# Kernel optimization log

Measured on AMD Instinct MI355X. Metric: run time of the kernel, lower is better.

The kernel has to match this reference:

```python
import jax, jax.numpy as jnp
import numpy as np

B = 4096          # graphs
NPG = 50          # nodes per graph
N = B * NPG       # total nodes
E = 819200        # edges
C = 128           # hidden_channels
T = 2048          # num_tools


def setup_inputs() -> dict:
    key = jax.random.key(0)
    ks = jax.random.split(key, 12)
    s = 0.1
    return {
        "x": jax.random.randint(ks[0], (N, 1), 0, T, dtype=jnp.int32),
        "edge_index": jax.random.randint(ks[1], (2, E), 0, N, dtype=jnp.int32),
        "batch": (jnp.arange(N, dtype=jnp.int32) // NPG).astype(jnp.int32),
        "num_graphs": B,
        "embedding": jax.random.normal(ks[2], (T, C), jnp.float32) * s,
        "w_ih": jax.random.normal(ks[3], (3 * C, C), jnp.float32) * s,
        "w_hh": jax.random.normal(ks[4], (3 * C, C), jnp.float32) * s,
        "w1": jax.random.normal(ks[5], (C, C), jnp.float32) * s,
        "w2": jax.random.normal(ks[6], (C, C), jnp.float32) * s,
        "b2": jax.random.normal(ks[7], (C,), jnp.float32) * s,
        "wq": jax.random.normal(ks[8], (C, C), jnp.float32) * s,
        "bq": jax.random.normal(ks[9], (C,), jnp.float32) * s,
        "wt": jax.random.normal(ks[10], (C, 2 * C), jnp.float32) * s,
    }


def reference(x, edge_index, batch, num_graphs, embedding, w_ih, w_hh,
              w1, w2, b2, wq, bq, wt):
    n = x.shape[0]
    # embedding lookup (dropout2d is identity at eval)
    emb = embedding[x[:, 0]]                                   # [N, C]

    # --- GatedGraphConv: scatter-add of source features to targets ---
    src, dst = edge_index[0], edge_index[1]
    m = jax.ops.segment_sum(emb[src], dst, num_segments=n)     # [N, C]

    # --- GRUCell(m, emb), no bias ---
    gi = m @ w_ih.T                                            # [N, 3C]
    gh = emb @ w_hh.T                                          # [N, 3C]
    i_r, i_z, i_n = jnp.split(gi, 3, axis=1)
    h_r, h_z, h_n = jnp.split(gh, 3, axis=1)
    r = jax.nn.sigmoid(i_r + h_r)
    z = jax.nn.sigmoid(i_z + h_z)
    ncand = jnp.tanh(i_n + r * h_n)
    h = (1.0 - z) * ncand + z * emb                            # [N, C]

    # --- ragged segment attention readout ---
    counts = jax.ops.segment_sum(jnp.ones_like(batch), batch,
                                 num_segments=num_graphs)      # [B]
    last_idx = jnp.cumsum(counts) - 1                          # [B]
    w_l = h[last_idx]                                          # [B, C] last node per graph
    w_g_r = w_l[batch]                                         # [N, C] broadcast to nodes
    q1 = w_g_r @ w1.T
    q2 = h @ w2.T + b2
    alpha = jax.nn.sigmoid(q1 + q2) @ wq.T + bq                # [N, C]
    w_g = jax.ops.segment_sum(alpha * h, batch,
                              num_segments=num_graphs)         # [B, C]

    w = jnp.concatenate([w_l, w_g], axis=1) @ wt.T             # [B, C]
    logits = w @ embedding.T                                   # [B, T]
    return logits
```

## Files before the change

kernel.cpp:

```cpp
#include <hip/hip_runtime.h>
#include <hip/hip_bf16.h>

#define NN 204800
#define EE 819200
#define BB 4096
#define NPG 50
#define CC 128
#define TT 2048
#define BINCAP 32

typedef __attribute__((ext_vector_type(8))) short short8;
typedef __attribute__((ext_vector_type(4))) float f32x4;

__device__ __forceinline__ short f2bf(float f) {
    union { float f; unsigned u; } v; v.f = f;
    unsigned r = (v.u + 0x7FFFu + ((v.u >> 16) & 1u)) >> 16;
    return (short)r;
}
__device__ __forceinline__ float bf2f(short s) {
    union { float f; unsigned u; } v;
    v.u = ((unsigned)(unsigned short)s) << 16;
    return v.f;
}
__device__ __forceinline__ float sigf(float x) { return 1.0f / (1.0f + __expf(-x)); }
__device__ __forceinline__ float tanh_fast(float x) {
    x = fminf(fmaxf(x, -15.0f), 15.0f);
    float e = __expf(2.0f * x);
    return 1.0f - 2.0f / (e + 1.0f);
}

__global__ void prep_small(const float* __restrict__ emb, const float* __restrict__ w1,
                           const float* __restrict__ w2, const float* __restrict__ wq,
                           const float* __restrict__ wt,
                           __hip_bfloat16* __restrict__ embbf, __hip_bfloat16* __restrict__ w1bf,
                           __hip_bfloat16* __restrict__ w2bf, __hip_bfloat16* __restrict__ wqbf,
                           __hip_bfloat16* __restrict__ wtbf) {
    int i = blockIdx.x * 256 + threadIdx.x;
    if (i < TT * CC) embbf[i] = __float2bfloat16(emb[i]);
    if (i < CC * CC) {
        w1bf[i] = __float2bfloat16(w1[i]);
        w2bf[i] = __float2bfloat16(w2[i]);
        wqbf[i] = __float2bfloat16(wq[i]);
    }
    if (i < CC * 2 * CC) wtbf[i] = __float2bfloat16(wt[i]);
}

__global__ __launch_bounds__(256) void build_tables(const float* __restrict__ emb,
                                                    const float* __restrict__ w_ih,
                                                    const float* __restrict__ w_hh,
                                                    __hip_bfloat16* __restrict__ G_ih,
                                                    __hip_bfloat16* __restrict__ G_hh) {
    __shared__ float wch[CC][CC + 1];
    __shared__ float et[16][CC];
    int t = threadIdx.x;
    int tokbase = blockIdx.x * 16;
    int chunk = blockIdx.y;
    const float* w = (chunk < 3) ? w_ih : w_hh;
    __hip_bfloat16* G = (chunk < 3) ? G_ih : G_hh;
    int jbase = (chunk % 3) * CC;
    for (int idx = t; idx < CC * CC; idx += 256) {
        int j = idx >> 7, k = idx & 127;
        wch[j][k] = w[(jbase + j) * CC + k];
    }
    for (int idx = t; idx < 16 * CC; idx += 256) {
        int tok = idx >> 7, k = idx & 127;
        et[tok][k] = emb[(tokbase + tok) * CC + k];
    }
    __syncthreads();
    int j = t & 127, grp = t >> 7;
    float acc[8];
#pragma unroll
    for (int u = 0; u < 8; u++) acc[u] = 0.f;
    for (int k = 0; k < CC; k++) {
        float wv = wch[j][k];
#pragma unroll
        for (int u = 0; u < 8; u++) acc[u] += et[grp * 8 + u][k] * wv;
    }
#pragma unroll
    for (int u = 0; u < 8; u++)
        G[(tokbase + grp * 8 + u) * 384 + jbase + j] = __float2bfloat16(acc[u]);
}

__global__ void fill_bins(const int* __restrict__ ei, const int* __restrict__ x,
                          int* __restrict__ deg, int* __restrict__ bins) {
    int e = blockIdx.x * 256 + threadIdx.x;
    int d = ei[EE + e], s = ei[e];
    int pos = atomicAdd(&deg[d], 1);
    bins[(size_t)d * BINCAP + pos] = x[s];
}

__global__ __launch_bounds__(256) void gru_kernel(
    const int* __restrict__ x, const int* __restrict__ deg,
    const int* __restrict__ bins,
    const __hip_bfloat16* __restrict__ G_ih, const __hip_bfloat16* __restrict__ G_hh,
    const float* __restrict__ emb,
    __hip_bfloat16* __restrict__ hbf) {
    int nid = blockIdx.x * 16 + (threadIdx.x >> 4);
    int j = threadIdx.x & 15;
    int tok = x[nid];
    int dg = deg[nid];
    const int* bin = bins + (size_t)nid * BINCAP;
    float ir[8], iz[8], inn[8];
#pragma unroll
    for (int p = 0; p < 8; p++) { ir[p] = 0.f; iz[p] = 0.f; inn[p] = 0.f; }
    for (int c = 0; c < dg; c += 4) {
        int4 tq = *(const int4*)&bin[c];
        int tks[4] = {tq.x, tq.y, tq.z, tq.w};
#pragma unroll
        for (int u = 0; u < 4; u++) {
            if (c + u < dg) {
                int st = tks[u];
                const short8* gp = (const short8*)(G_ih + (size_t)st * 384);
                short8 a = gp[j];
                short8 b = gp[16 + j];
                short8 c2 = gp[32 + j];
#pragma unroll
                for (int p = 0; p < 8; p++) {
                    ir[p]  += bf2f(a[p]);
                    iz[p]  += bf2f(b[p]);
                    inn[p] += bf2f(c2[p]);
                }
            }
        }
    }
    const short8* hp = (const short8*)(G_hh + (size_t)tok * 384);
    short8 hr = hp[j], hz = hp[16 + j], hn = hp[32 + j];
    const float4* ep = (const float4*)(emb + (size_t)tok * CC + j * 8);
    float4 ev0 = ep[0], ev1 = ep[1];
    float evs[8] = {ev0.x, ev0.y, ev0.z, ev0.w, ev1.x, ev1.y, ev1.z, ev1.w};
    short8 hv;
#pragma unroll
    for (int p = 0; p < 8; p++) {
        float r  = sigf(ir[p] + bf2f(hr[p]));
        float z  = sigf(iz[p] + bf2f(hz[p]));
        float nc = tanh_fast(inn[p] + r * bf2f(hn[p]));
        float h  = (1.f - z) * nc + z * evs[p];
        hv[p] = f2bf(h);
    }
    ((short8*)hbf)[nid * 16 + j] = hv;
}

__global__ __launch_bounds__(256) void q1_kernel(
    const __hip_bfloat16* __restrict__ hbf, const __hip_bfloat16* __restrict__ w1bf,
    const float* __restrict__ b2,
    float* __restrict__ q1_all, __hip_bfloat16* __restrict__ w_lbf) {
    int t = threadIdx.x;
    int gbase = blockIdx.x * 64;
    int wave = t >> 6, lane = t & 63;
    int mrow = lane & 15, quad = lane >> 4;
    int g = gbase + wave * 16 + mrow;

    short8 afr[4];
#pragma unroll
    for (int kt = 0; kt < 4; kt++) {
        afr[kt] = *(const short8*)(hbf + ((size_t)g * NPG + NPG - 1) * CC + kt * 32 + quad * 8);
        *(short8*)(w_lbf + (size_t)g * CC + kt * 32 + quad * 8) = afr[kt];
    }
    f32x4 acc[8];
#pragma unroll
    for (int nt = 0; nt < 8; nt++) {
        float bv = b2[nt * 16 + mrow];
        acc[nt] = (f32x4){bv, bv, bv, bv};
    }
#pragma unroll
    for (int kt = 0; kt < 4; kt++) {
#pragma unroll
        for (int nt = 0; nt < 8; nt++) {
            const short8* bp = (const short8*)(w1bf + (nt * 16 + mrow) * CC + kt * 32 + quad * 8);
            acc[nt] = __builtin_amdgcn_mfma_f32_16x16x32_bf16(afr[kt], *bp, acc[nt], 0, 0, 0);
        }
    }
#pragma unroll
    for (int nt = 0; nt < 8; nt++)
#pragma unroll
        for (int r = 0; r < 4; r++)
            q1_all[(size_t)(gbase + wave * 16 + quad * 4 + r) * CC + nt * 16 + mrow] = acc[nt][r];
}

__global__ __launch_bounds__(256, 4) void node_attn(
    const __hip_bfloat16* __restrict__ hbf, const float* __restrict__ q1_all,
    const __hip_bfloat16* __restrict__ w2bf, const __hip_bfloat16* __restrict__ wqbf,
    const float* __restrict__ bq,
    float* __restrict__ w_gf) {
    __shared__ short hsb[64][CC + 8];
    __shared__ short ssb[64][CC + 8];
    int rb = blockIdx.x * 64;
    int t = threadIdx.x;

    const short8* hsrc = (const short8*)(hbf + (size_t)rb * CC);
#pragma unroll
    for (int it = 0; it < 4; it++) {
        int idx = it * 256 + t;
        *(short8*)&hsb[idx >> 4][(idx & 15) * 8] = hsrc[idx];
    }
    __syncthreads();

    int wave = t >> 6, lane = t & 63;
    int mrow = lane & 15, quad = lane >> 4;
    int colb = wave * 32;

    f32x4 acc[4][2];
#pragma unroll
    for (int rt = 0; rt < 4; rt++)
#pragma unroll
        for (int n = 0; n < 2; n++) acc[rt][n] = (f32x4){0.f, 0.f, 0.f, 0.f};
    {
        short8 bw2[2][4];
#pragma unroll
        for (int n = 0; n < 2; n++)
#pragma unroll
            for (int kt = 0; kt < 4; kt++)
                bw2[n][kt] = *(const short8*)(w2bf + (size_t)(colb + n * 16 + mrow) * CC + kt * 32 + quad * 8);
#pragma unroll
        for (int kt = 0; kt < 4; kt++)
#pragma unroll
            for (int rt = 0; rt < 4; rt++) {
                short8 af = *(const short8*)&hsb[rt * 16 + mrow][kt * 32 + quad * 8];
#pragma unroll
                for (int n = 0; n < 2; n++)
                    acc[rt][n] = __builtin_amdgcn_mfma_f32_16x16x32_bf16(af, bw2[n][kt], acc[rt][n], 0, 0, 0);
            }
    }
#pragma unroll
    for (int rt = 0; rt < 4; rt++)
#pragma unroll
        for (int n = 0; n < 2; n++)
#pragma unroll
            for (int r = 0; r < 4; r++) {
                int rowl = rt * 16 + quad * 4 + r;
                int col = colb + n * 16 + mrow;
                int g = (rb + rowl) / 50;
                ssb[rowl][col] = f2bf(sigf(acc[rt][n][r] + q1_all[(size_t)g * CC + col]));
            }
    __syncthreads();

    f32x4 acd[4][2];
    short8 bwq[2][4];
#pragma unroll
    for (int n = 0; n < 2; n++) {
        float bv = bq[colb + n * 16 + mrow];
#pragma unroll
        for (int rt = 0; rt < 4; rt++) acd[rt][n] = (f32x4){bv, bv, bv, bv};
#pragma unroll
        for (int kt = 0; kt < 4; kt++)
            bwq[n][kt] = *(const short8*)(wqbf + (size_t)(colb + n * 16 + mrow) * CC + kt * 32 + quad * 8);
    }
#pragma unroll
    for (int kt = 0; kt < 4; kt++)
#pragma unroll
        for (int rt = 0; rt < 4; rt++) {
            short8 af = *(const short8*)&ssb[rt * 16 + mrow][kt * 32 + quad * 8];
#pragma unroll
            for (int n = 0; n < 2; n++)
                acd[rt][n] = __builtin_amdgcn_mfma_f32_16x16x32_bf16(af, bwq[n][kt], acd[rt][n], 0, 0, 0);
        }
    int g0 = rb / 50;
    int gmax = (rb + 63) / 50;
#pragma unroll
    for (int n = 0; n < 2; n++) {
        int col = colb + n * 16 + mrow;
        float ps0 = 0.f, ps1 = 0.f, ps2 = 0.f;
#pragma unroll
        for (int rt = 0; rt < 4; rt++)
#pragma unroll
            for (int r = 0; r < 4; r++) {
                int rowl = rt * 16 + quad * 4 + r;
                int gg = (rb + rowl) / 50;
                float v = acd[rt][n][r] * bf2f(hsb[rowl][col]);
                ps0 += (gg == g0)     ? v : 0.f;
                ps1 += (gg == g0 + 1) ? v : 0.f;
                ps2 += (gg == g0 + 2) ? v : 0.f;
            }
        ps0 += __shfl_xor(ps0, 16, 64); ps0 += __shfl_xor(ps0, 32, 64);
        ps1 += __shfl_xor(ps1, 16, 64); ps1 += __shfl_xor(ps1, 32, 64);
        ps2 += __shfl_xor(ps2, 16, 64); ps2 += __shfl_xor(ps2, 32, 64);
        if (quad == 0) {
            atomicAdd(&w_gf[(size_t)g0 * CC + col], ps0);
            if (g0 + 1 <= gmax) atomicAdd(&w_gf[(size_t)(g0 + 1) * CC + col], ps1);
            if (g0 + 2 <= gmax) atomicAdd(&w_gf[(size_t)(g0 + 2) * CC + col], ps2);
        }
    }
}

__global__ __launch_bounds__(256) void wvec_kernel(
    const __hip_bfloat16* __restrict__ w_lbf, const float* __restrict__ w_gf,
    const __hip_bfloat16* __restrict__ wtbf,
    __hip_bfloat16* __restrict__ wvecbf) {
    int t = threadIdx.x;
    int gbase = blockIdx.x * 64;
    int wave = t >> 6, lane = t & 63;
    int mrow = lane & 15, quad = lane >> 4;
    int grow = gbase + wave * 16 + mrow;

    f32x4 acc[8];
#pragma unroll
    for (int nt = 0; nt < 8; nt++) acc[nt] = (f32x4){0.f, 0.f, 0.f, 0.f};
#pragma unroll
    for (int kt = 0; kt < 8; kt++) {
        short8 af;
        if (kt < 4) {
            af = *(const short8*)(w_lbf + (size_t)grow * CC + kt * 32 + quad * 8);
        } else {
            const float* ws = w_gf + (size_t)grow * CC + (kt - 4) * 32 + quad * 8;
            float4 v0 = *(const float4*)ws, v1 = *(const float4*)(ws + 4);
            af[0] = f2bf(v0.x); af[1] = f2bf(v0.y); af[2] = f2bf(v0.z); af[3] = f2bf(v0.w);
            af[4] = f2bf(v1.x); af[5] = f2bf(v1.y); af[6] = f2bf(v1.z); af[7] = f2bf(v1.w);
        }
#pragma unroll
        for (int nt = 0; nt < 8; nt++) {
            const short8* bp = (const short8*)(wtbf + (nt * 16 + mrow) * 256 + kt * 32 + quad * 8);
            acc[nt] = __builtin_amdgcn_mfma_f32_16x16x32_bf16(af, *bp, acc[nt], 0, 0, 0);
        }
    }
#pragma unroll
    for (int nt = 0; nt < 8; nt++)
#pragma unroll
        for (int r = 0; r < 4; r++)
            wvecbf[(size_t)(gbase + wave * 16 + quad * 4 + r) * CC + nt * 16 + mrow] =
                __float2bfloat16(acc[nt][r]);
}

__global__ __launch_bounds__(256) void logits_kernel(
    const __hip_bfloat16* __restrict__ wvecbf, const __hip_bfloat16* __restrict__ embbf,
    float* __restrict__ out) {
    __shared__ short avs[64][CC + 8];
    int t = threadIdx.x;
    int gbase = blockIdx.x * 64;
    int tbase = blockIdx.y * 128;

    const short8* asrc = (const short8*)(wvecbf + (size_t)gbase * CC);
#pragma unroll
    for (int it = 0; it < 4; it++) {
        int idx = it * 256 + t;
        *(short8*)&avs[idx >> 4][(idx & 15) * 8] = asrc[idx];
    }
    __syncthreads();

    int wave = t >> 6, lane = t & 63;
    int mrow = lane & 15, quad = lane >> 4;

    f32x4 acc3[8];
#pragma unroll
    for (int nt = 0; nt < 8; nt++) acc3[nt] = (f32x4){0.f, 0.f, 0.f, 0.f};
#pragma unroll
    for (int kt = 0; kt < 4; kt++) {
        short8 af = *(const short8*)&avs[wave * 16 + mrow][kt * 32 + quad * 8];
#pragma unroll
        for (int nt = 0; nt < 8; nt++) {
            const short8* bp = (const short8*)(embbf + (size_t)(tbase + nt * 16 + mrow) * CC + kt * 32 + quad * 8);
            acc3[nt] = __builtin_amdgcn_mfma_f32_16x16x32_bf16(af, *bp, acc3[nt], 0, 0, 0);
        }
    }
#pragma unroll
    for (int nt = 0; nt < 8; nt++)
#pragma unroll
        for (int r = 0; r < 4; r++) {
            int grow2 = gbase + wave * 16 + quad * 4 + r;
            int tok = tbase + nt * 16 + mrow;
            out[(size_t)grow2 * TT + tok] = acc3[nt][r];
        }
}

extern "C" void kernel_launch(void* const* d_in, const int* in_sizes, int n_in,
                              void* d_out, int out_size, void* d_ws, size_t ws_size,
                              hipStream_t stream) {
    const int* x     = (const int*)d_in[0];
    const int* ei    = (const int*)d_in[1];
    const float* emb = (const float*)d_in[4];
    const float* w_ih = (const float*)d_in[5];
    const float* w_hh = (const float*)d_in[6];
    const float* w1  = (const float*)d_in[7];
    const float* w2  = (const float*)d_in[8];
    const float* b2  = (const float*)d_in[9];
    const float* wq  = (const float*)d_in[10];
    const float* bq  = (const float*)d_in[11];
    const float* wt  = (const float*)d_in[12];
    float* out = (float*)d_out;

    char* ws = (char*)d_ws;
    size_t off = 0;
    auto alloc = [&](size_t b) { void* p = ws + off; off += (b + 255) & ~(size_t)255; return p; };
    __hip_bfloat16* G_ih  = (__hip_bfloat16*)alloc((size_t)TT * 384 * 2);
    __hip_bfloat16* G_hh  = (__hip_bfloat16*)alloc((size_t)TT * 384 * 2);
    __hip_bfloat16* embbf = (__hip_bfloat16*)alloc((size_t)TT * CC * 2);
    __hip_bfloat16* w1bf  = (__hip_bfloat16*)alloc((size_t)CC * CC * 2);
    __hip_bfloat16* w2bf  = (__hip_bfloat16*)alloc((size_t)CC * CC * 2);
    __hip_bfloat16* wqbf  = (__hip_bfloat16*)alloc((size_t)CC * CC * 2);
    __hip_bfloat16* wtbf  = (__hip_bfloat16*)alloc((size_t)CC * 256 * 2);
    int* deg              = (int*)alloc((size_t)NN * 4);
    int* bins             = (int*)alloc((size_t)NN * BINCAP * 4);
    __hip_bfloat16* w_lbf = (__hip_bfloat16*)alloc((size_t)BB * CC * 2);
    float* w_gf           = (float*)alloc((size_t)BB * CC * 4);
    float* q1_all         = (float*)alloc((size_t)BB * CC * 4);
    __hip_bfloat16* wvecbf= (__hip_bfloat16*)alloc((size_t)BB * CC * 2);
    __hip_bfloat16* hbf   = (__hip_bfloat16*)alloc((size_t)NN * CC * 2);

    hipMemsetAsync(deg, 0, (size_t)NN * 4, stream);
    hipMemsetAsync(w_gf, 0, (size_t)BB * CC * 4, stream);
    prep_small<<<1024, 256, 0, stream>>>(emb, w1, w2, wq, wt, embbf, w1bf, w2bf, wqbf, wtbf);
    build_tables<<<dim3(TT / 16, 6), 256, 0, stream>>>(emb, w_ih, w_hh, G_ih, G_hh);
    fill_bins<<<EE / 256, 256, 0, stream>>>(ei, x, deg, bins);
    gru_kernel<<<NN / 16, 256, 0, stream>>>(x, deg, bins, G_ih, G_hh, emb, hbf);
    q1_kernel<<<BB / 64, 256, 0, stream>>>(hbf, w1bf, b2, q1_all, w_lbf);
    node_attn<<<NN / 64, 256, 0, stream>>>(hbf, q1_all, w2bf, wqbf, bq, w_gf);
    wvec_kernel<<<BB / 64, 256, 0, stream>>>(w_lbf, w_gf, wtbf, wvecbf);
    logits_kernel<<<dim3(BB / 64, TT / 128), 256, 0, stream>>>(wvecbf, embbf, out);
}
```

Before: 308.8 us.

## Build GRU tables with MFMA, branchless gather, and cache q1 in LDS

Replaces the scalar fp32 FMA kernel that builds the per-token GRU gate tables with a bf16 MFMA kernel. The weights and embeddings are converted to bf16 in prep_small first. The GRU gather loop becomes branchless by pointing out-of-range slots at an extra zeroed table row. node_attn stages the three relevant q1 rows and each node's graph index in shared memory instead of doing per-element global loads and divisions. Table precision drops from an fp32 dot product to bf16 inputs, and the launch order changes.

Result: no change. 304.3 us (-1.5%).

```diff
diff --git a/kernel.cpp b/kernel.cpp
--- a/kernel.cpp
+++ b/kernel.cpp
@@ -31,10 +31,12 @@
 
 __global__ void prep_small(const float* __restrict__ emb, const float* __restrict__ w1,
                            const float* __restrict__ w2, const float* __restrict__ wq,
-                           const float* __restrict__ wt,
+                           const float* __restrict__ wt, const float* __restrict__ w_ih,
+                           const float* __restrict__ w_hh,
                            __hip_bfloat16* __restrict__ embbf, __hip_bfloat16* __restrict__ w1bf,
                            __hip_bfloat16* __restrict__ w2bf, __hip_bfloat16* __restrict__ wqbf,
-                           __hip_bfloat16* __restrict__ wtbf) {
+                           __hip_bfloat16* __restrict__ wtbf, __hip_bfloat16* __restrict__ w_ihbf,
+                           __hip_bfloat16* __restrict__ w_hhbf) {
     int i = blockIdx.x * 256 + threadIdx.x;
     if (i < TT * CC) embbf[i] = __float2bfloat16(emb[i]);
     if (i < CC * CC) {
@@ -43,42 +45,65 @@
         wqbf[i] = __float2bfloat16(wq[i]);
     }
     if (i < CC * 2 * CC) wtbf[i] = __float2bfloat16(wt[i]);
-}
-
-__global__ __launch_bounds__(256) void build_tables(const float* __restrict__ emb,
-                                                    const float* __restrict__ w_ih,
-                                                    const float* __restrict__ w_hh,
-                                                    __hip_bfloat16* __restrict__ G_ih,
-                                                    __hip_bfloat16* __restrict__ G_hh) {
-    __shared__ float wch[CC][CC + 1];
-    __shared__ float et[16][CC];
+    if (i < 3 * CC * CC) {
+        w_ihbf[i] = __float2bfloat16(w_ih[i]);
+        w_hhbf[i] = __float2bfloat16(w_hh[i]);
+    }
+}
+
+__global__ __launch_bounds__(256) void build_tables_mfma(
+    const __hip_bfloat16* __restrict__ embbf,
+    const __hip_bfloat16* __restrict__ w_ihbf, const __hip_bfloat16* __restrict__ w_hhbf,
+    __hip_bfloat16* __restrict__ G_ih, __hip_bfloat16* __restrict__ G_hh) {
+    __shared__ short at[64][CC + 8];
     int t = threadIdx.x;
-    int tokbase = blockIdx.x * 16;
+    int tokbase = blockIdx.x * 64;
     int chunk = blockIdx.y;
-    const float* w = (chunk < 3) ? w_ih : w_hh;
+    const __hip_bfloat16* wsel = (chunk < 3) ? w_ihbf : w_hhbf;
     __hip_bfloat16* G = (chunk < 3) ? G_ih : G_hh;
     int jbase = (chunk % 3) * CC;
-    for (int idx = t; idx < CC * CC; idx += 256) {
-        int j = idx >> 7, k = idx & 127;
-        wch[j][k] = w[(jbase + j) * CC + k];
-    }
-    for (int idx = t; idx < 16 * CC; idx += 256) {
-        int tok = idx >> 7, k = idx & 127;
-        et[tok][k] = emb[(tokbase + tok) * CC + k];
+
+    const short8* asrc = (const short8*)(embbf + (size_t)tokbase * CC);
+#pragma unroll
+    for (int it = 0; it < 4; it++) {
+        int idx = it * 256 + t;
+        *(short8*)&at[idx >> 4][(idx & 15) * 8] = asrc[idx];
     }
     __syncthreads();
-    int j = t & 127, grp = t >> 7;
-    float acc[8];
-#pragma unroll
-    for (int u = 0; u < 8; u++) acc[u] = 0.f;
-    for (int k = 0; k < CC; k++) {
-        float wv = wch[j][k];
-#pragma unroll
-        for (int u = 0; u < 8; u++) acc[u] += et[grp * 8 + u][k] * wv;
-    }
-#pragma unroll
-    for (int u = 0; u < 8; u++)
-        G[(tokbase + grp * 8 + u) * 384 + jbase + j] = __float2bfloat16(acc[u]);
+
+    int wave = t >> 6, lane = t & 63;
+    int mrow = lane & 15, quad = lane >> 4;
+    int colb = wave * 32;
+
+    f32x4 acc[4][2];
+#pragma unroll
+    for (int rt = 0; rt < 4; rt++)
+#pragma unroll
+        for (int n = 0; n < 2; n++) acc[rt][n] = (f32x4){0.f, 0.f, 0.f, 0.f};
+    short8 bw[2][4];
+#pragma unroll
+    for (int n = 0; n < 2; n++)
+#pragma unroll
+        for (int kt = 0; kt < 4; kt++)
+            bw[n][kt] = *(const short8*)(wsel + (size_t)(jbase + colb + n * 16 + mrow) * CC + kt * 32 + quad * 8);
+#pragma unroll
+    for (int kt = 0; kt < 4; kt++)
+#pragma unroll
+        for (int rt = 0; rt < 4; rt++) {
+            short8 af = *(const short8*)&at[rt * 16 + mrow][kt * 32 + quad * 8];
+#pragma unroll
+            for (int n = 0; n < 2; n++)
+                acc[rt][n] = __builtin_amdgcn_mfma_f32_16x16x32_bf16(af, bw[n][kt], acc[rt][n], 0, 0, 0);
+        }
+#pragma unroll
+    for (int rt = 0; rt < 4; rt++)
+#pragma unroll
+        for (int n = 0; n < 2; n++)
+#pragma unroll
+            for (int r = 0; r < 4; r++) {
+                int tok = tokbase + rt * 16 + quad * 4 + r;
+                G[(size_t)tok * 384 + jbase + colb + n * 16 + mrow] = __float2bfloat16(acc[rt][n][r]);
+            }
 }
 
 __global__ void fill_bins(const int* __restrict__ ei, const int* __restrict__ x,
@@ -108,18 +133,16 @@
         int tks[4] = {tq.x, tq.y, tq.z, tq.w};
 #pragma unroll
         for (int u = 0; u < 4; u++) {
-            if (c + u < dg) {
-                int st = tks[u];
-                const short8* gp = (const short8*)(G_ih + (size_t)st * 384);
-                short8 a = gp[j];
-                short8 b = gp[16 + j];
-                short8 c2 = gp[32 + j];
-#pragma unroll
-                for (int p = 0; p < 8; p++) {
-                    ir[p]  += bf2f(a[p]);
-                    iz[p]  += bf2f(b[p]);
-                    inn[p] += bf2f(c2[p]);
-                }
+            int st = (c + u < dg) ? tks[u] : TT;
+            const short8* gp = (const short8*)(G_ih + (size_t)st * 384);
+            short8 a = gp[j];
+            short8 b = gp[16 + j];
+            short8 c2 = gp[32 + j];
+#pragma unroll
+            for (int p = 0; p < 8; p++) {
+                ir[p]  += bf2f(a[p]);
+                iz[p]  += bf2f(b[p]);
+                inn[p] += bf2f(c2[p]);
             }
         }
     }
@@ -184,7 +207,10 @@
     float* __restrict__ w_gf) {
     __shared__ short hsb[64][CC + 8];
     __shared__ short ssb[64][CC + 8];
+    __shared__ float q1s[3][CC];
+    __shared__ int gidx[64];
     int rb = blockIdx.x * 64;
+    int g0 = rb / 50;
     int t = threadIdx.x;
 
     const short8* hsrc = (const short8*)(hbf + (size_t)rb * CC);
@@ -193,6 +219,11 @@
         int idx = it * 256 + t;
         *(short8*)&hsb[idx >> 4][(idx & 15) * 8] = hsrc[idx];
     }
+    if (t < 64) gidx[t] = (rb + t) / 50 - g0;
+    for (int idx = t; idx < 3 * CC; idx += 256) {
+        int gg = g0 + (idx >> 7);
+        q1s[idx >> 7][idx & 127] = (gg < BB) ? q1_all[(size_t)gg * CC + (idx & 127)] : 0.f;
+    }
     __syncthreads();
 
     int wave = t >> 6, lane = t & 63;
@@ -224,14 +255,15 @@
 #pragma unroll
     for (int rt = 0; rt < 4; rt++)
 #pragma unroll
-        for (int n = 0; n < 2; n++)
-#pragma unroll
-            for (int r = 0; r < 4; r++) {
-                int rowl = rt * 16 + quad * 4 + r;
+        for (int r = 0; r < 4; r++) {
+            int rowl = rt * 16 + quad * 4 + r;
+            int gi_ = gidx[rowl];
+#pragma unroll
+            for (int n = 0; n < 2; n++) {
                 int col = colb + n * 16 + mrow;
-                int g = (rb + rowl) / 50;
-                ssb[rowl][col] = f2bf(sigf(acc[rt][n][r] + q1_all[(size_t)g * CC + col]));
+                ssb[rowl][col] = f2bf(sigf(acc[rt][n][r] + q1s[gi_][col]));
             }
+        }
     __syncthreads();
 
     f32x4 acd[4][2];
@@ -254,8 +286,6 @@
             for (int n = 0; n < 2; n++)
                 acd[rt][n] = __builtin_amdgcn_mfma_f32_16x16x32_bf16(af, bwq[n][kt], acd[rt][n], 0, 0, 0);
         }
-    int g0 = rb / 50;
-    int gmax = (rb + 63) / 50;
 #pragma unroll
     for (int n = 0; n < 2; n++) {
         int col = colb + n * 16 + mrow;
@@ -265,19 +295,19 @@
 #pragma unroll
             for (int r = 0; r < 4; r++) {
                 int rowl = rt * 16 + quad * 4 + r;
-                int gg = (rb + rowl) / 50;
+                int gi_ = gidx[rowl];
                 float v = acd[rt][n][r] * bf2f(hsb[rowl][col]);
-                ps0 += (gg == g0)     ? v : 0.f;
-                ps1 += (gg == g0 + 1) ? v : 0.f;
-                ps2 += (gg == g0 + 2) ? v : 0.f;
+                ps0 += (gi_ == 0) ? v : 0.f;
+                ps1 += (gi_ == 1) ? v : 0.f;
+                ps2 += (gi_ == 2) ? v : 0.f;
             }
         ps0 += __shfl_xor(ps0, 16, 64); ps0 += __shfl_xor(ps0, 32, 64);
         ps1 += __shfl_xor(ps1, 16, 64); ps1 += __shfl_xor(ps1, 32, 64);
         ps2 += __shfl_xor(ps2, 16, 64); ps2 += __shfl_xor(ps2, 32, 64);
         if (quad == 0) {
             atomicAdd(&w_gf[(size_t)g0 * CC + col], ps0);
-            if (g0 + 1 <= gmax) atomicAdd(&w_gf[(size_t)(g0 + 1) * CC + col], ps1);
-            if (g0 + 2 <= gmax) atomicAdd(&w_gf[(size_t)(g0 + 2) * CC + col], ps2);
+            atomicAdd(&w_gf[(size_t)(g0 + 1) * CC + col], ps1);
+            if (g0 + 2 < BB) atomicAdd(&w_gf[(size_t)(g0 + 2) * CC + col], ps2);
         }
     }
 }
@@ -380,13 +410,15 @@
     char* ws = (char*)d_ws;
     size_t off = 0;
     auto alloc = [&](size_t b) { void* p = ws + off; off += (b + 255) & ~(size_t)255; return p; };
-    __hip_bfloat16* G_ih  = (__hip_bfloat16*)alloc((size_t)TT * 384 * 2);
+    __hip_bfloat16* G_ih  = (__hip_bfloat16*)alloc((size_t)(TT + 1) * 384 * 2);
     __hip_bfloat16* G_hh  = (__hip_bfloat16*)alloc((size_t)TT * 384 * 2);
     __hip_bfloat16* embbf = (__hip_bfloat16*)alloc((size_t)TT * CC * 2);
     __hip_bfloat16* w1bf  = (__hip_bfloat16*)alloc((size_t)CC * CC * 2);
     __hip_bfloat16* w2bf  = (__hip_bfloat16*)alloc((size_t)CC * CC * 2);
     __hip_bfloat16* wqbf  = (__hip_bfloat16*)alloc((size_t)CC * CC * 2);
     __hip_bfloat16* wtbf  = (__hip_bfloat16*)alloc((size_t)CC * 256 * 2);
+    __hip_bfloat16* w_ihbf= (__hip_bfloat16*)alloc((size_t)3 * CC * CC * 2);
+    __hip_bfloat16* w_hhbf= (__hip_bfloat16*)alloc((size_t)3 * CC * CC * 2);
     int* deg              = (int*)alloc((size_t)NN * 4);
     int* bins             = (int*)alloc((size_t)NN * BINCAP * 4);
     __hip_bfloat16* w_lbf = (__hip_bfloat16*)alloc((size_t)BB * CC * 2);
@@ -397,9 +429,11 @@
 
     hipMemsetAsync(deg, 0, (size_t)NN * 4, stream);
     hipMemsetAsync(w_gf, 0, (size_t)BB * CC * 4, stream);
-    prep_small<<<1024, 256, 0, stream>>>(emb, w1, w2, wq, wt, embbf, w1bf, w2bf, wqbf, wtbf);
-    build_tables<<<dim3(TT / 16, 6), 256, 0, stream>>>(emb, w_ih, w_hh, G_ih, G_hh);
+    hipMemsetAsync(G_ih + (size_t)TT * 384, 0, 384 * 2, stream);
     fill_bins<<<EE / 256, 256, 0, stream>>>(ei, x, deg, bins);
+    prep_small<<<1024, 256, 0, stream>>>(emb, w1, w2, wq, wt, w_ih, w_hh,
+                                         embbf, w1bf, w2bf, wqbf, wtbf, w_ihbf, w_hhbf);
+    build_tables_mfma<<<dim3(TT / 64, 6), 256, 0, stream>>>(embbf, w_ihbf, w_hhbf, G_ih, G_hh);
     gru_kernel<<<NN / 16, 256, 0, stream>>>(x, deg, bins, G_ih, G_hh, emb, hbf);
     q1_kernel<<<BB / 64, 256, 0, stream>>>(hbf, w1bf, b2, q1_all, w_lbf);
     node_attn<<<NN / 64, 256, 0, stream>>>(hbf, q1_all, w2bf, wqbf, bq, w_gf);
```
